# Kernel optimization log

Measured on AMD Instinct MI355X. Metric: run time of the kernel, lower is better.

Reference implementation:

```python
import jax, jax.numpy as jnp
import numpy as np

B, S, H, NH = 2, 2048, 4096, 32
HD = H // NH  # 128
ROPE_THETA = 10000.0
SCALE = HD ** -0.5


def _rope_neox(x, positions):
    # x: [B,S,NH,HD]; positions: [B,S] int32. NEOX-style (half split) rotary.
    half = HD // 2
    inv_freq = ROPE_THETA ** (-jnp.arange(0, half, dtype=jnp.float32) / half)
    freqs = positions.astype(jnp.float32)[..., None] * inv_freq  # [B,S,half]
    cos = jnp.cos(freqs)[:, :, None, :]  # [B,S,1,half]
    sin = jnp.sin(freqs)[:, :, None, :]
    x1, x2 = x[..., :half], x[..., half:]
    return jnp.concatenate([x1 * cos - x2 * sin, x2 * cos + x1 * sin], axis=-1)


def setup_inputs() -> dict:
    key = jax.random.key(0)
    k1, k2, k3, k4 = jax.random.split(key, 4)
    positions = jnp.tile(jnp.arange(S, dtype=jnp.int32)[None, :], (B, 1))
    hidden_states = jax.random.normal(k1, (B, S, H), dtype=jnp.float32)
    W_qkv = jax.random.normal(k2, (H, 3 * H), dtype=jnp.float32) * (H ** -0.5)
    b_qkv = jax.random.normal(k3, (3 * H,), dtype=jnp.float32) * 0.02
    W_o = jax.random.normal(k4, (H, H), dtype=jnp.float32) * (H ** -0.5)
    return {"positions": positions, "hidden_states": hidden_states,
            "W_qkv": W_qkv, "b_qkv": b_qkv, "W_o": W_o}


def reference(positions, hidden_states, W_qkv, b_qkv, W_o):
    qkv = jnp.einsum('bsh,hf->bsf', hidden_states, W_qkv) + b_qkv  # [B,S,3H]
    q, k, v = jnp.split(qkv, 3, axis=-1)
    q = q.reshape(B, S, NH, HD)
    k = k.reshape(B, S, NH, HD)
    v = v.reshape(B, S, NH, HD)
    q = _rope_neox(q, positions)
    k = _rope_neox(k, positions)
    # causal attention (RadixAttention prefill, num_kv_heads == num_heads)
    scores = jnp.einsum('bqhd,bkhd->bhqk', q, k) * SCALE  # [B,NH,S,S]
    causal = jnp.tril(jnp.ones((S, S), dtype=bool))
    scores = jnp.where(causal[None, None], scores, jnp.finfo(scores.dtype).min)
    probs = jax.nn.softmax(scores, axis=-1)
    attn = jnp.einsum('bhqk,bkhd->bqhd', probs, v).reshape(B, S, H)
    return jnp.einsum('bsh,ho->bso', attn, W_o)
```

## Files before the change

kernel.cpp:

```cpp
#include <hip/hip_runtime.h>
#include <hip/hip_bf16.h>

#define B_ 2
#define S_ 2048
#define H_ 4096
#define NH_ 32
#define HD_ 128
#define M_TOK (B_*S_)
#define N_QKV (3*H_)
#define SCALE_ 0.08838834764831845f

using bf16 = __hip_bfloat16;
typedef __attribute__((ext_vector_type(8))) short bf16x8;
typedef __attribute__((ext_vector_type(4))) float f32x4;

typedef __attribute__((address_space(1))) const void global_cvoid;
typedef __attribute__((address_space(3))) void lds_void;

__device__ __forceinline__ void async_ld16(const void* g, void* l) {
  __builtin_amdgcn_global_load_lds((global_cvoid*)g, (lds_void*)l, 16, 0, 0);
}

__device__ __forceinline__ unsigned short bf_bits(float x) {
  bf16 h = __float2bfloat16(x);
  return *reinterpret_cast<unsigned short*>(&h);
}


__global__ void cast_bf16_kernel(const float* __restrict__ in, bf16* __restrict__ out) {
  size_t i = ((size_t)blockIdx.x*256 + threadIdx.x)*4;
  float4 v = *(const float4*)(in + i);
  struct alignas(8) B4 { bf16 a,b,c,d; } t;
  t.a = __float2bfloat16(v.x); t.b = __float2bfloat16(v.y);
  t.c = __float2bfloat16(v.z); t.d = __float2bfloat16(v.w);
  *(B4*)(out + i) = t;
}

__global__ void transpose_cast_kernel(const float* __restrict__ in, bf16* __restrict__ out,
                                      int R, int C) {
  __shared__ float tile[32][33];
  int c0 = blockIdx.x*32, r0 = blockIdx.y*32;
  int tx = threadIdx.x, ty = threadIdx.y;
#pragma unroll
  for (int i = 0; i < 4; ++i)
    tile[ty + i*8][tx] = in[(size_t)(r0 + ty + i*8)*C + c0 + tx];
  __syncthreads();
#pragma unroll
  for (int i = 0; i < 4; ++i)
    out[(size_t)(c0 + ty + i*8)*R + r0 + tx] = __float2bfloat16(tile[tx][ty + i*8]);
}

__global__ void transpose_v_kernel(const bf16* __restrict__ in, bf16* __restrict__ out) {
  __shared__ bf16 tile[32][33];
  int bh = blockIdx.z;
  int d0 = blockIdx.x*32, s0 = blockIdx.y*32;
  int tx = threadIdx.x, ty = threadIdx.y;
#pragma unroll
  for (int i = 0; i < 4; ++i)
    tile[ty + i*8][tx] = in[((size_t)bh*S_ + s0 + ty + i*8)*HD_ + d0 + tx];
  __syncthreads();
#pragma unroll
  for (int i = 0; i < 4; ++i)
    out[((size_t)bh*HD_ + d0 + ty + i*8)*S_ + s0 + tx] = tile[tx][ty + i*8];
}

__global__ void rope_kernel(bf16* __restrict__ q, bf16* __restrict__ k,
                            const int* __restrict__ pos) {
  size_t idx = (size_t)blockIdx.x*256 + threadIdx.x;
  int d = idx & 63;
  size_t r1 = idx >> 6;
  int s = (int)(r1 & (S_-1));
  int bh = (int)(r1 >> 11);
  int b = bh >> 5;
  int p = pos[b*S_ + s];
  float inv = exp2f(-0.2076205059304660f * (float)d);
  float ang = (float)p * inv;
  float sn, cs;
  __sincosf(ang, &sn, &cs);
  size_t base = ((size_t)bh*S_ + s)*HD_ + d;
  float x1 = __bfloat162float(q[base]), x2 = __bfloat162float(q[base+64]);
  q[base]    = __float2bfloat16(x1*cs - x2*sn);
  q[base+64] = __float2bfloat16(x2*cs + x1*sn);
  float y1 = __bfloat162float(k[base]), y2 = __bfloat162float(k[base+64]);
  k[base]    = __float2bfloat16(y1*cs - y2*sn);
  k[base+64] = __float2bfloat16(y2*cs + y1*sn);
}

template<int EPI>
__global__ __launch_bounds__(256)
void gemm_bt_kernel(const bf16* __restrict__ A, const bf16* __restrict__ Bt,
                    const float* __restrict__ bias, float* __restrict__ Cf,
                    bf16* __restrict__ qb, bf16* __restrict__ kb, bf16* __restrict__ vb,
                    int M, int N, int K)
{
  __shared__ unsigned short As[128*64];
  __shared__ unsigned short Bs[128*64];
  const int tid = threadIdx.x;
  const int wave = tid >> 6, lane = tid & 63;
  const int l15 = lane & 15, l4 = lane >> 4;
  const int bn = blockIdx.x, bm = blockIdx.y;
  const int m0 = bm*128, n0 = bn*128;
  const int wr = wave >> 1, wc = wave & 1;

  const bf16* ga = A  + (size_t)(m0 + wave*32 + (lane>>3))*K + (lane&7)*8;
  const bf16* gb = Bt + (size_t)(n0 + wave*32 + (lane>>3))*K + (lane&7)*8;
  unsigned short* lA = As + wave*32*64;
  unsigned short* lB = Bs + wave*32*64;

  f32x4 acc[4][4] = {};

  for (int kt = 0; kt < K; kt += 64) {
    __syncthreads();
#pragma unroll
    for (int j = 0; j < 4; ++j) {
      async_ld16(ga + kt + (size_t)j*8*K, lA + j*8*64);
      async_ld16(gb + kt + (size_t)j*8*K, lB + j*8*64);
    }
    asm volatile("s_waitcnt vmcnt(0)" ::: "memory");
    __syncthreads();
#pragma unroll
    for (int kk = 0; kk < 2; ++kk) {
      bf16x8 af[4], bfr[4];
#pragma unroll
      for (int mi = 0; mi < 4; ++mi)
        af[mi] = *(const bf16x8*)(As + (size_t)(wr*64 + mi*16 + l15)*64 + kk*32 + l4*8);
#pragma unroll
      for (int ni = 0; ni < 4; ++ni)
        bfr[ni] = *(const bf16x8*)(Bs + (size_t)(wc*64 + ni*16 + l15)*64 + kk*32 + l4*8);
#pragma unroll
      for (int mi = 0; mi < 4; ++mi)
#pragma unroll
        for (int ni = 0; ni < 4; ++ni)
          acc[mi][ni] = __builtin_amdgcn_mfma_f32_16x16x32_bf16(af[mi], bfr[ni], acc[mi][ni], 0, 0, 0);
    }
  }

#pragma unroll
  for (int mi = 0; mi < 4; ++mi) {
#pragma unroll
    for (int ni = 0; ni < 4; ++ni) {
      int n = n0 + wc*64 + ni*16 + l15;
#pragma unroll
      for (int r = 0; r < 4; ++r) {
        int m = m0 + wr*64 + mi*16 + l4*4 + r;
        float v = acc[mi][ni][r];
        if (EPI == 0) {
          v += bias[n];
          int which = n >> 12;
          int h = (n >> 7) & 31;
          int d = n & 127;
          int b = m >> 11, s = m & (S_-1);
          bf16* dst = (which == 0) ? qb : (which == 1) ? kb : vb;
          dst[((size_t)(b*NH_ + h)*S_ + s)*HD_ + d] = __float2bfloat16(v);
        } else {
          Cf[(size_t)m*N + n] = v;
        }
      }
    }
  }
}

__global__ __launch_bounds__(256)
void flash_kernel(const bf16* __restrict__ q, const bf16* __restrict__ k,
                  const bf16* __restrict__ vt, bf16* __restrict__ o)
{
  __shared__ unsigned short Ks[64*136];
  __shared__ unsigned short Vts[128*72];
  __shared__ unsigned short Ps[4*16*72];
  const int tid = threadIdx.x;
  const int wave = tid >> 6, lane = tid & 63;
  const int l15 = lane & 15, l4 = lane >> 4;
  const int qt = blockIdx.x;
  const int bh = blockIdx.y;
  const int q0 = qt*64 + wave*16;

  bf16x8 qf[4];
#pragma unroll
  for (int kk = 0; kk < 4; ++kk)
    qf[kk] = *(const bf16x8*)(q + ((size_t)bh*S_ + q0 + l15)*HD_ + kk*32 + l4*8);

  f32x4 oacc[8] = {};
  float mst[4], lst[4];
#pragma unroll
  for (int r = 0; r < 4; ++r) { mst[r] = -1e30f; lst[r] = 0.f; }

  unsigned short* Pw = Ps + wave*16*72;

  for (int t = 0; t <= qt; ++t) {
    const int kv0 = t*64;
    __syncthreads();
#pragma unroll
    for (int i = 0; i < 4; ++i) {
      int c = tid + i*256;
      int row = c >> 4, cc = c & 15;
      *(int4*)(Ks + (size_t)row*136 + cc*8) =
        *(const int4*)(k + ((size_t)bh*S_ + kv0 + row)*HD_ + cc*8);
    }
#pragma unroll
    for (int i = 0; i < 4; ++i) {
      int c = tid + i*256;
      int row = c >> 3, cc = c & 7;
      *(int4*)(Vts + (size_t)row*72 + cc*8) =
        *(const int4*)(vt + ((size_t)bh*HD_ + row)*S_ + kv0 + cc*8);
    }
    __syncthreads();

    f32x4 sacc[4] = {};
#pragma unroll
    for (int kk = 0; kk < 4; ++kk) {
#pragma unroll
      for (int ni = 0; ni < 4; ++ni) {
        bf16x8 kf = *(const bf16x8*)(Ks + (size_t)(ni*16 + l15)*136 + kk*32 + l4*8);
        sacc[ni] = __builtin_amdgcn_mfma_f32_16x16x32_bf16(qf[kk], kf, sacc[ni], 0, 0, 0);
      }
    }
    float sv[4][4];
    float rmax[4];
#pragma unroll
    for (int r = 0; r < 4; ++r) rmax[r] = -1e30f;
#pragma unroll
    for (int ni = 0; ni < 4; ++ni) {
      int kv = kv0 + ni*16 + l15;
#pragma unroll
      for (int r = 0; r < 4; ++r) {
        int qrow = q0 + l4*4 + r;
        float x = sacc[ni][r] * SCALE_;
        if (kv > qrow) x = -1e30f;
        sv[ni][r] = x;
        rmax[r] = fmaxf(rmax[r], x);
      }
    }
#pragma unroll
    for (int mm = 1; mm < 16; mm <<= 1)
#pragma unroll
      for (int r = 0; r < 4; ++r)
        rmax[r] = fmaxf(rmax[r], __shfl_xor(rmax[r], mm));
    float fac[4], rsum[4];
#pragma unroll
    for (int r = 0; r < 4; ++r) {
      float mn = fmaxf(mst[r], rmax[r]);
      fac[r] = __expf(mst[r] - mn);
      mst[r] = mn;
      rsum[r] = 0.f;
    }
#pragma unroll
    for (int ni = 0; ni < 4; ++ni) {
#pragma unroll
      for (int r = 0; r < 4; ++r) {
        float p = __expf(sv[ni][r] - mst[r]);
        rsum[r] += p;
        Pw[(size_t)(l4*4 + r)*72 + ni*16 + l15] = bf_bits(p);
      }
    }
#pragma unroll
    for (int mm = 1; mm < 16; mm <<= 1)
#pragma unroll
      for (int r = 0; r < 4; ++r)
        rsum[r] += __shfl_xor(rsum[r], mm);
#pragma unroll
    for (int r = 0; r < 4; ++r)
      lst[r] = lst[r]*fac[r] + rsum[r];
#pragma unroll
    for (int nd = 0; nd < 8; ++nd)
#pragma unroll
      for (int r = 0; r < 4; ++r)
        oacc[nd][r] *= fac[r];
    bf16x8 pa[2];
#pragma unroll
    for (int kk = 0; kk < 2; ++kk)
      pa[kk] = *(const bf16x8*)(Pw + (size_t)l15*72 + kk*32 + l4*8);
#pragma unroll
    for (int nd = 0; nd < 8; ++nd) {
#pragma unroll
      for (int kk = 0; kk < 2; ++kk) {
        bf16x8 vf = *(const bf16x8*)(Vts + (size_t)(nd*16 + l15)*72 + kk*32 + l4*8);
        oacc[nd] = __builtin_amdgcn_mfma_f32_16x16x32_bf16(pa[kk], vf, oacc[nd], 0, 0, 0);
      }
    }
  }

  int b = bh >> 5, h = bh & 31;
  float invl[4];
#pragma unroll
  for (int r = 0; r < 4; ++r) invl[r] = 1.f / lst[r];
#pragma unroll
  for (int nd = 0; nd < 8; ++nd)
#pragma unroll
    for (int r = 0; r < 4; ++r) {
      int qrow = q0 + l4*4 + r;
      o[((size_t)(b*S_ + qrow))*H_ + h*HD_ + nd*16 + l15] =
        __float2bfloat16(oacc[nd][r] * invl[r]);
    }
}


extern "C" void kernel_launch(void* const* d_in, const int* in_sizes, int n_in,
                              void* d_out, int out_size, void* d_ws, size_t ws_size,
                              hipStream_t stream)
{
  const int*   positions = (const int*)d_in[0];
  const float* hidden    = (const float*)d_in[1];
  const float* Wqkv      = (const float*)d_in[2];
  const float* bqkv      = (const float*)d_in[3];
  const float* Wo        = (const float*)d_in[4];
  float* out = (float*)d_out;

  char* ws = (char*)d_ws;
  const size_t MB = 1024*1024;
  bf16* hs16    = (bf16*)(ws);
  bf16* wqkvT   = (bf16*)(ws + 32*MB);
  bf16* woT     = (bf16*)(ws + 128*MB);
  bf16* qbuf    = (bf16*)(ws + 160*MB);
  bf16* kbuf    = (bf16*)(ws + 192*MB);
  bf16* vbuf    = (bf16*)(ws + 224*MB);
  bf16* vtbuf   = (bf16*)(ws + 256*MB);
  bf16* attnbuf = hs16;

  cast_bf16_kernel<<<dim3((M_TOK*(size_t)H_)/1024), dim3(256), 0, stream>>>(hidden, hs16);
  transpose_cast_kernel<<<dim3(N_QKV/32, H_/32), dim3(32,8), 0, stream>>>(Wqkv, wqkvT, H_, N_QKV);
  transpose_cast_kernel<<<dim3(H_/32, H_/32), dim3(32,8), 0, stream>>>(Wo, woT, H_, H_);

  gemm_bt_kernel<0><<<dim3(N_QKV/128, M_TOK/128), dim3(256), 0, stream>>>(
      hs16, wqkvT, bqkv, nullptr, qbuf, kbuf, vbuf, M_TOK, N_QKV, H_);

  rope_kernel<<<dim3((B_*NH_*S_*64)/256), dim3(256), 0, stream>>>(qbuf, kbuf, positions);

  transpose_v_kernel<<<dim3(HD_/32, S_/32, B_*NH_), dim3(32,8), 0, stream>>>(vbuf, vtbuf);

  flash_kernel<<<dim3(S_/64, B_*NH_), dim3(256), 0, stream>>>(qbuf, kbuf, vtbuf, attnbuf);

  gemm_bt_kernel<1><<<dim3(H_/128, M_TOK/128), dim3(256), 0, stream>>>(
      attnbuf, woT, nullptr, out, nullptr, nullptr, nullptr, M_TOK, H_, H_);
}
```

Before: 1.663 ms.

## Replace GEMM with 256x256 tile, 8-wave double-buffered pipelined kernel

Replaces the simple 128x128 single-buffered GEMM with a 256x256 tile kernel using 8 waves. It double-buffers swizzled LDS tiles and interleaves the async global-to-LDS loads for the next K step with MFMA on the current one. It also remaps workgroup IDs to improve L2 locality and raises MFMA wave priority. The aim is to hide memory latency and avoid LDS bank conflicts in both projection GEMMs. In exchange the code uses 128KB of LDS and relies on a careful barrier/waitcnt schedule.

New measurement: 1.364 ms. 18.0% less time.

```diff
diff --git a/kernel.cpp b/kernel.cpp
--- a/kernel.cpp
+++ b/kernel.cpp
@@ -86,75 +86,130 @@
   k[base+64] = __float2bfloat16(y2*cs + y1*sn);
 }
 
+
+#define BAR __builtin_amdgcn_s_barrier()
+#define LGKM0 do{ asm volatile("s_waitcnt lgkmcnt(0)":::"memory"); __builtin_amdgcn_sched_barrier(0);}while(0)
+#define VMW(N) asm volatile("s_waitcnt vmcnt(" #N ")":::"memory")
+
+#define LOAD_AF(HALF) do{ const unsigned short* Ab=&As[db][HALF][0]; \
+  _Pragma("unroll") for(int mi=0;mi<4;++mi) _Pragma("unroll") for(int kk=0;kk<2;++kk) \
+    af[mi][kk] = *(const bf16x8*)(Ab + (wr*64+mi*16+l15)*64 + (((kk*4+l4)^sw)<<3)); }while(0)
+
+#define LOAD_BF(DEST,HALF) do{ const unsigned short* Bb=&Bs[db][HALF][0]; \
+  _Pragma("unroll") for(int ni=0;ni<2;++ni) _Pragma("unroll") for(int kk=0;kk<2;++kk) \
+    DEST[ni][kk] = *(const bf16x8*)(Bb + (wc*32+ni*16+l15)*64 + (((kk*4+l4)^sw)<<3)); }while(0)
+
+#define MFMA16(QM,QN,BQ) do{ __builtin_amdgcn_s_setprio(1); \
+  _Pragma("unroll") for(int mi=0;mi<4;++mi) _Pragma("unroll") for(int ni=0;ni<2;++ni) \
+    _Pragma("unroll") for(int kk=0;kk<2;++kk) \
+      acc[QM][QN][mi][ni] = __builtin_amdgcn_mfma_f32_16x16x32_bf16(af[mi][kk], BQ[ni][kk], acc[QM][QN][mi][ni],0,0,0); \
+  __builtin_amdgcn_s_setprio(0); }while(0)
+
 template<int EPI>
-__global__ __launch_bounds__(256)
-void gemm_bt_kernel(const bf16* __restrict__ A, const bf16* __restrict__ Bt,
-                    const float* __restrict__ bias, float* __restrict__ Cf,
-                    bf16* __restrict__ qb, bf16* __restrict__ kb, bf16* __restrict__ vb,
-                    int M, int N, int K)
+__global__ __launch_bounds__(512, 2)
+void gemm8_kernel(const bf16* __restrict__ A, const bf16* __restrict__ Bt,
+                  const float* __restrict__ bias, float* __restrict__ Cf,
+                  bf16* __restrict__ qb, bf16* __restrict__ kb, bf16* __restrict__ vb,
+                  int M, int N, int K)
 {
-  __shared__ unsigned short As[128*64];
-  __shared__ unsigned short Bs[128*64];
+  __shared__ alignas(16) unsigned short As[2][2][128*64];
+  __shared__ alignas(16) unsigned short Bs[2][2][128*64];
+
   const int tid = threadIdx.x;
   const int wave = tid >> 6, lane = tid & 63;
   const int l15 = lane & 15, l4 = lane >> 4;
-  const int bn = blockIdx.x, bm = blockIdx.y;
-  const int m0 = bm*128, n0 = bn*128;
-  const int wr = wave >> 1, wc = wave & 1;
-
-  const bf16* ga = A  + (size_t)(m0 + wave*32 + (lane>>3))*K + (lane&7)*8;
-  const bf16* gb = Bt + (size_t)(n0 + wave*32 + (lane>>3))*K + (lane&7)*8;
-  unsigned short* lA = As + wave*32*64;
-  unsigned short* lB = Bs + wave*32*64;
-
-  f32x4 acc[4][4] = {};
-
-  for (int kt = 0; kt < K; kt += 64) {
-    __syncthreads();
-#pragma unroll
-    for (int j = 0; j < 4; ++j) {
-      async_ld16(ga + kt + (size_t)j*8*K, lA + j*8*64);
-      async_ld16(gb + kt + (size_t)j*8*K, lB + j*8*64);
-    }
-    asm volatile("s_waitcnt vmcnt(0)" ::: "memory");
-    __syncthreads();
-#pragma unroll
-    for (int kk = 0; kk < 2; ++kk) {
-      bf16x8 af[4], bfr[4];
-#pragma unroll
-      for (int mi = 0; mi < 4; ++mi)
-        af[mi] = *(const bf16x8*)(As + (size_t)(wr*64 + mi*16 + l15)*64 + kk*32 + l4*8);
-#pragma unroll
-      for (int ni = 0; ni < 4; ++ni)
-        bfr[ni] = *(const bf16x8*)(Bs + (size_t)(wc*64 + ni*16 + l15)*64 + kk*32 + l4*8);
-#pragma unroll
-      for (int mi = 0; mi < 4; ++mi)
-#pragma unroll
-        for (int ni = 0; ni < 4; ++ni)
-          acc[mi][ni] = __builtin_amdgcn_mfma_f32_16x16x32_bf16(af[mi], bfr[ni], acc[mi][ni], 0, 0, 0);
-    }
+  const int sw = l15 & 7;
+  const int wr = wave >> 2, wc = wave & 3;
+
+  const int gn = N >> 8;
+  const int nwg = gridDim.x;
+  const int orig = blockIdx.x;
+  const int wg = (orig & 7)*(nwg >> 3) + (orig >> 3);
+  const int bm = wg / gn, bn = wg % gn;
+  const int m0 = bm*256, n0 = bn*256;
+  const int NT = K >> 6;
+
+  auto stA = [&](int buf, int h, int koff) {
+#pragma unroll
+    for (int j = 0; j < 2; ++j) {
+      int ci = (j << 9) + tid;
+      int row = ci >> 3;
+      int sl = (ci & 7) ^ (row & 7);
+      async_ld16(A + (size_t)(m0 + h*128 + row)*K + koff + sl*8, &As[buf][h][ci*8]);
+    }
+  };
+  auto stB = [&](int buf, int h, int koff) {
+#pragma unroll
+    for (int j = 0; j < 2; ++j) {
+      int ci = (j << 9) + tid;
+      int row = ci >> 3;
+      int sl = (ci & 7) ^ (row & 7);
+      async_ld16(Bt + (size_t)(n0 + h*128 + row)*K + koff + sl*8, &Bs[buf][h][ci*8]);
+    }
+  };
+
+  f32x4 acc[2][2][4][2] = {};
+  bf16x8 af[4][2], bq0[2][2], bq1[2][2];
+
+  stA(0,0,0); stB(0,0,0); stA(0,1,0); stB(0,1,0); stA(1,0,64); stB(1,0,64);
+  VMW(8); BAR;
+
+  for (int t = 0; t < NT-1; ++t) {
+    const int db = t & 1;
+    LOAD_AF(0); LOAD_BF(bq0,0);
+    stA(db^1, 1, (t+1)*64);
+    BAR; LGKM0; MFMA16(0,0,bq0);
+    VMW(6); BAR;
+    LOAD_BF(bq1,1);
+    stB(db^1, 1, (t+1)*64);
+    BAR; LGKM0; MFMA16(0,1,bq1);
+    BAR;
+    LOAD_AF(1);
+    if (t+2 < NT) stA(db, 0, (t+2)*64);
+    BAR; LGKM0; MFMA16(1,0,bq0);
+    BAR;
+    if (t+2 < NT) stB(db, 0, (t+2)*64);
+    BAR; MFMA16(1,1,bq1);
+    if (t+2 < NT) { VMW(8); } else { VMW(4); }
+    BAR;
   }
-
-#pragma unroll
-  for (int mi = 0; mi < 4; ++mi) {
-#pragma unroll
-    for (int ni = 0; ni < 4; ++ni) {
-      int n = n0 + wc*64 + ni*16 + l15;
-#pragma unroll
-      for (int r = 0; r < 4; ++r) {
-        int m = m0 + wr*64 + mi*16 + l4*4 + r;
-        float v = acc[mi][ni][r];
-        if (EPI == 0) {
-          v += bias[n];
-          int which = n >> 12;
-          int h = (n >> 7) & 31;
-          int d = n & 127;
-          int b = m >> 11, s = m & (S_-1);
-          bf16* dst = (which == 0) ? qb : (which == 1) ? kb : vb;
-          dst[((size_t)(b*NH_ + h)*S_ + s)*HD_ + d] = __float2bfloat16(v);
-        } else {
-          Cf[(size_t)m*N + n] = v;
-        }
+  {
+    const int db = (NT-1) & 1;
+    LOAD_AF(0); LOAD_BF(bq0,0);
+    BAR; LGKM0; MFMA16(0,0,bq0);
+    VMW(0); BAR;
+    LOAD_BF(bq1,1);
+    BAR; LGKM0; MFMA16(0,1,bq1);
+    BAR;
+    LOAD_AF(1);
+    BAR; LGKM0; MFMA16(1,0,bq0);
+    BAR;
+    MFMA16(1,1,bq1);
+  }
+
+#pragma unroll
+  for (int qm = 0; qm < 2; ++qm)
+#pragma unroll
+  for (int qn = 0; qn < 2; ++qn)
+#pragma unroll
+  for (int mi = 0; mi < 4; ++mi)
+#pragma unroll
+  for (int ni = 0; ni < 2; ++ni) {
+    int n = n0 + qn*128 + wc*32 + ni*16 + l15;
+#pragma unroll
+    for (int r = 0; r < 4; ++r) {
+      int m = m0 + qm*128 + wr*64 + mi*16 + l4*4 + r;
+      float v = acc[qm][qn][mi][ni][r];
+      if (EPI == 0) {
+        v += bias[n];
+        int which = n >> 12;
+        int h = (n >> 7) & 31;
+        int d = n & 127;
+        int b = m >> 11, s = m & (S_-1);
+        bf16* dst = (which == 0) ? qb : (which == 1) ? kb : vb;
+        dst[((size_t)(b*NH_ + h)*S_ + s)*HD_ + d] = __float2bfloat16(v);
+      } else {
+        Cf[(size_t)m*N + n] = v;
       }
     }
   }
@@ -320,7 +375,7 @@
   transpose_cast_kernel<<<dim3(N_QKV/32, H_/32), dim3(32,8), 0, stream>>>(Wqkv, wqkvT, H_, N_QKV);
   transpose_cast_kernel<<<dim3(H_/32, H_/32), dim3(32,8), 0, stream>>>(Wo, woT, H_, H_);
 
-  gemm_bt_kernel<0><<<dim3(N_QKV/128, M_TOK/128), dim3(256), 0, stream>>>(
+  gemm8_kernel<0><<<dim3((M_TOK/256)*(N_QKV/256)), dim3(512), 0, stream>>>(
       hs16, wqkvT, bqkv, nullptr, qbuf, kbuf, vbuf, M_TOK, N_QKV, H_);
 
   rope_kernel<<<dim3((B_*NH_*S_*64)/256), dim3(256), 0, stream>>>(qbuf, kbuf, positions);
@@ -329,6 +384,6 @@
 
   flash_kernel<<<dim3(S_/64, B_*NH_), dim3(256), 0, stream>>>(qbuf, kbuf, vtbuf, attnbuf);
 
-  gemm_bt_kernel<1><<<dim3(H_/128, M_TOK/128), dim3(256), 0, stream>>>(
+  gemm8_kernel<1><<<dim3((M_TOK/256)*(H_/256)), dim3(512), 0, stream>>>(
       attnbuf, woT, nullptr, out, nullptr, nullptr, nullptr, M_TOK, H_, H_);
 }
```
